# Performance work log

Hardware: AMD Instinct MI355X
Metric: run time of the kernel (lower is better)

## Reference

```python
import jax, jax.numpy as jnp
import numpy as np

HOP = 512
FAC = 4
FRAME_LEN = FAC * HOP  # 2048
ALPHA = 0.65
BETA = 0.06


def _inverse_stft_window():
    # torch.hann_window (periodic): w[n] = 0.5*(1 - cos(2*pi*n/N))
    n = np.arange(FRAME_LEN)
    w = 0.5 * (1.0 - np.cos(2.0 * np.pi * n / FRAME_LEN))
    denom = w ** 2
    # overlaps = ceil(frame_length / hop) == FAC (frame_length = FAC*HOP exactly)
    denom = denom.reshape(FAC, HOP).sum(axis=0)          # [HOP]
    denom = np.tile(denom, FAC)                          # [FRAME_LEN]
    return (w / denom).astype(np.float32)


def setup_inputs() -> dict:
    key = jax.random.key(0)
    B, F, T = 8, 1024, 2048
    stft_frames = jax.random.normal(key, (B, 2, F, T), dtype=jnp.float32)
    inv_window = jnp.asarray(_inverse_stft_window())
    return {"stft_frames": stft_frames, "inv_window": inv_window}


def reference(stft_frames, inv_window):
    # stft_frames: [B, 2, F, T] (real/imag stacked on dim 1)
    x = jnp.pad(stft_frames, ((0, 0), (0, 0), (0, 1), (0, 0)))  # F -> F+1 (Nyquist bin)
    real = x[:, 0] / BETA   # [B, F+1, T]
    imag = x[:, 1] / BETA
    # denormalize_complex: |x|^(1/alpha) * exp(i * atan2(im, re))
    mag = (real * real + imag * imag) ** (0.5 / ALPHA)
    theta = jnp.arctan2(imag, real)
    spec = jax.lax.complex(mag * jnp.cos(theta), mag * jnp.sin(theta))  # [B, F+1, T]
    frames = jnp.fft.irfft(spec, axis=-2)                 # [B, 2F, T], 2F == FRAME_LEN
    frames = jnp.transpose(frames, (0, 2, 1))             # [B, T, L]
    frames = frames * inv_window[None, None, :]
    B, T, L = frames.shape
    total = (T - 1) * HOP + L
    # vectorized overlap-add (scatter-add replacing the per-frame python loop)
    idx = (jnp.arange(T)[:, None] * HOP + jnp.arange(L)[None, :]).reshape(-1)  # [T*L]
    full = jnp.zeros((B, total), frames.dtype).at[:, idx].add(frames.reshape(B, -1))
    # output_buffer is empty on the first call; chunk = first hop*T samples
    return full[:, : HOP * T]
```

## Files before the change

kernel.cpp:

```cpp
#include <hip/hip_runtime.h>
#include <cstddef>


#define TDIM 2048
#define FDIM 1024
#define TT 8
#define NTOT (512 * 2048)
#define SPLANE 4224

static constexpr int kBREV[32] = {0,16,8,24,4,20,12,28,2,18,10,26,6,22,14,30,
                                  1,17,9,25,5,21,13,29,3,19,11,27,7,23,15,31};
static constexpr float kTR[16] = {
  1.0f, 0.98078528040323044f, 0.92387953251128674f, 0.83146961230254524f,
  0.70710678118654757f, 0.55557023301960218f, 0.38268343236508978f, 0.19509032201612825f,
  0.0f, -0.19509032201612825f, -0.38268343236508978f, -0.55557023301960218f,
  -0.70710678118654757f, -0.83146961230254524f, -0.92387953251128674f, -0.98078528040323044f};
static constexpr float kTI[16] = {
  0.0f, 0.19509032201612825f, 0.38268343236508978f, 0.55557023301960218f,
  0.70710678118654757f, 0.83146961230254524f, 0.92387953251128674f, 0.98078528040323044f,
  1.0f, 0.98078528040323044f, 0.92387953251128674f, 0.83146961230254524f,
  0.70710678118654757f, 0.55557023301960218f, 0.38268343236508978f, 0.19509032201612825f};
static constexpr float kCC[32] = {
  1.0f, 0.99518472667219693f, 0.98078528040323044f, 0.95694033573220882f,
  0.92387953251128674f, 0.88192126434835505f, 0.83146961230254524f, 0.77301045336273699f,
  0.70710678118654757f, 0.63439328416364549f, 0.55557023301960218f, 0.47139673682599764f,
  0.38268343236508978f, 0.29028467725446233f, 0.19509032201612825f, 0.098017140329560604f,
  0.0f, -0.098017140329560604f, -0.19509032201612825f, -0.29028467725446233f,
  -0.38268343236508978f, -0.47139673682599764f, -0.55557023301960218f, -0.63439328416364549f,
  -0.70710678118654757f, -0.77301045336273699f, -0.83146961230254524f, -0.88192126434835505f,
  -0.92387953251128674f, -0.95694033573220882f, -0.98078528040323044f, -0.99518472667219693f};
static constexpr float kSS[32] = {
  0.0f, 0.098017140329560604f, 0.19509032201612825f, 0.29028467725446233f,
  0.38268343236508978f, 0.47139673682599764f, 0.55557023301960218f, 0.63439328416364549f,
  0.70710678118654757f, 0.77301045336273699f, 0.83146961230254524f, 0.88192126434835505f,
  0.92387953251128674f, 0.95694033573220882f, 0.98078528040323044f, 0.99518472667219693f,
  1.0f, 0.99518472667219693f, 0.98078528040323044f, 0.95694033573220882f,
  0.92387953251128674f, 0.88192126434835505f, 0.83146961230254524f, 0.77301045336273699f,
  0.70710678118654757f, 0.63439328416364549f, 0.55557023301960218f, 0.47139673682599764f,
  0.38268343236508978f, 0.29028467725446233f, 0.19509032201612825f, 0.098017140329560604f};

template <int H>
__device__ __forceinline__ void fft32_stage(float ar[32], float ai[32]) {
  constexpr int TSTEP = 16 / H;
  #pragma unroll
  for (int g = 0; g < 32; g += 2 * H) {
    #pragma unroll
    for (int j = 0; j < H; ++j) {
      const float twr = kTR[j * TSTEP];
      const float twi = kTI[j * TSTEP];
      const int i0 = g + j, i1 = i0 + H;
      const float tr = twr * ar[i1] - twi * ai[i1];
      const float ti = twr * ai[i1] + twi * ar[i1];
      ar[i1] = ar[i0] - tr; ai[i1] = ai[i0] - ti;
      ar[i0] += tr;         ai[i0] += ti;
    }
  }
}

__device__ __forceinline__ void ifft32_core(float ar[32], float ai[32]) {
  fft32_stage<1>(ar, ai);
  fft32_stage<2>(ar, ai);
  fft32_stage<4>(ar, ai);
  fft32_stage<8>(ar, ai);
  fft32_stage<16>(ar, ai);
}

__device__ __forceinline__ float pow_gain(float v, float PE, float KS) {
  return KS * __builtin_amdgcn_exp2f(PE * __builtin_amdgcn_logf(v));
}

__device__ __forceinline__ void denorm4(float4& r, float4& i, float PE, float KS) {
  float g;
  g = pow_gain(r.x * r.x + i.x * i.x, PE, KS); r.x *= g; i.x *= g;
  g = pow_gain(r.y * r.y + i.y * i.y, PE, KS); r.y *= g; i.y *= g;
  g = pow_gain(r.z * r.z + i.z * i.z, PE, KS); r.z *= g; i.z *= g;
  g = pow_gain(r.w * r.w + i.w * i.w, PE, KS); r.w *= g; i.w *= g;
}

template <int SC>
__device__ __forceinline__ int slot_row(int s) {
  return (SC == 0) ? (s < 256 ? s : s + 512) : (s + 256);
}

template <int SC>
__device__ __forceinline__ void stage1_compute(const float* __restrict__ Sre,
                                               const float* __restrict__ Sim,
                                               int q, int tl, float wc, float ws,
                                               float ar[32], float ai[32]) {
  #pragma unroll
  for (int u = 0; u < 16; ++u) {
    const int k2 = (SC == 0) ? (u < 8 ? u : u + 16) : (u + 8);
    const int slot = q + 32 * u;
    int slotm_zero = 32 * (16 - u);
    if (SC == 0 && u == 0) slotm_zero = 0;
    if (SC == 0 && u == 8) slotm_zero = 512;
    const int slotm_pos = (32 - q) + 32 * (15 - u);
    const int slotm = (q == 0) ? slotm_zero : slotm_pos;

    const float s1r = Sre[slot * 8 + tl],  s1i = Sim[slot * 8 + tl];
    const float s2r = Sre[slotm * 8 + tl], s2i = Sim[slotm * 8 + tl];
    const float cs = wc * kCC[k2] - ws * kSS[k2];
    const float sn = ws * kCC[k2] + wc * kSS[k2];
    const float Pre = s1r + s2r, Pim = s1i - s2i;
    const float Qre = s1r - s2r, Qim = s1i + s2i;
    const float uu = cs * Qim + sn * Qre;
    const float vv = cs * Qre - sn * Qim;
    float wr = Pre - uu, wi = Pim + vv;
    if (q == 0 && k2 == 0) { wr = s1r; wi = s1r; }
    ar[kBREV[k2]] = wr; ai[kBREV[k2]] = wi;
  }
}

#define XH(t, k1, rh) ((k1) * 132 + (rh) * 8 + (t))
#define FSTR 2053

__global__ __launch_bounds__(256) void istft_fused(const float* __restrict__ in,
                                                   const float* __restrict__ invw,
                                                   float* __restrict__ out) {
  __shared__ float buf[8448];
  float* Sre = buf;
  float* Sim = buf + SPLANE;
  float* Xhr = buf;
  float* Xhi = buf + 4224;
  float* Fh  = buf;

  const int tid = threadIdx.x;
  const int tl  = tid & 7;
  const int q   = tid >> 3;

  const int id   = blockIdx.x;
  const int xcd  = id & 7;
  const int slot = id >> 3;
  const int b    = slot >> 5;
  const int tile = xcd * 32 + (slot & 31);
  const int t0   = tile * TT;

  const float* re_p = in + ((size_t)b * 2 + 0) * ((size_t)FDIM * TDIM);
  const float* im_p = in + ((size_t)b * 2 + 1) * ((size_t)FDIM * TDIM);

  const float KS = (float)(exp((-1.0 / 0.65) * log(0.06)) / 2048.0);
  const float PE = 7.0f / 26.0f;

  const float aq = 3.0679615757712824e-3f * (float)q;
  const float wc = __cosf(aq), ws = __sinf(aq);

  float ar[32], ai[32];

  float4 reA[4], imA[4];
  #pragma unroll
  for (int j = 0; j < 4; ++j) {
    const int f = tid + 256 * j;
    const int s = f >> 1, cg = f & 1;
    const int row = slot_row<0>(s);
    reA[j] = *(const float4*)(re_p + (size_t)row * TDIM + t0 + 4 * cg);
    imA[j] = *(const float4*)(im_p + (size_t)row * TDIM + t0 + 4 * cg);
  }
  float4 exRe, exIm;
  if (tid < 2) {
    exRe = *(const float4*)(re_p + (size_t)256 * TDIM + t0 + 4 * tid);
    exIm = *(const float4*)(im_p + (size_t)256 * TDIM + t0 + 4 * tid);
  }
  #pragma unroll
  for (int j = 0; j < 4; ++j) {
    const int f = tid + 256 * j;
    const int s = f >> 1, cg = f & 1;
    denorm4(reA[j], imA[j], PE, KS);
    *(float4*)(Sre + s * 8 + 4 * cg) = reA[j];
    *(float4*)(Sim + s * 8 + 4 * cg) = imA[j];
  }
  if (tid < 2) {
    denorm4(exRe, exIm, PE, KS);
    *(float4*)(Sre + 512 * 8 + 4 * tid) = exRe;
    *(float4*)(Sim + 512 * 8 + 4 * tid) = exIm;
  }

  float4 reB[4], imB[4];
  #pragma unroll
  for (int j = 0; j < 4; ++j) {
    const int f = tid + 256 * j;
    const int s = f >> 1, cg = f & 1;
    const int row = slot_row<1>(s);
    reB[j] = *(const float4*)(re_p + (size_t)row * TDIM + t0 + 4 * cg);
    imB[j] = *(const float4*)(im_p + (size_t)row * TDIM + t0 + 4 * cg);
  }
  float4 exReB, exImB;
  if (tid < 2) {
    exReB = *(const float4*)(re_p + (size_t)768 * TDIM + t0 + 4 * tid);
    exImB = *(const float4*)(im_p + (size_t)768 * TDIM + t0 + 4 * tid);
  }
  __syncthreads();

  stage1_compute<0>(Sre, Sim, q, tl, wc, ws, ar, ai);
  __syncthreads();

  #pragma unroll
  for (int j = 0; j < 4; ++j) {
    const int f = tid + 256 * j;
    const int s = f >> 1, cg = f & 1;
    denorm4(reB[j], imB[j], PE, KS);
    *(float4*)(Sre + s * 8 + 4 * cg) = reB[j];
    *(float4*)(Sim + s * 8 + 4 * cg) = imB[j];
  }
  if (tid < 2) {
    denorm4(exReB, exImB, PE, KS);
    *(float4*)(Sre + 512 * 8 + 4 * tid) = exReB;
    *(float4*)(Sim + 512 * 8 + 4 * tid) = exImB;
  }
  __syncthreads();
  stage1_compute<1>(Sre, Sim, q, tl, wc, ws, ar, ai);
  __syncthreads();

  ifft32_core(ar, ai);

  float zr[32], zi[32];
  #pragma unroll
  for (int r = 0; r < 16; ++r) {
    const float ang = 6.1359231515425649e-3f * (float)(q * r);
    const float sn = __sinf(ang), cs = __cosf(ang);
    Xhr[XH(tl, q, r)] = cs * ar[r] - sn * ai[r];
    Xhi[XH(tl, q, r)] = cs * ai[r] + sn * ar[r];
  }
  __syncthreads();
  if (q < 16) {
    #pragma unroll
    for (int i = 0; i < 32; ++i) {
      zr[i] = Xhr[XH(tl, kBREV[i], q)];
      zi[i] = Xhi[XH(tl, kBREV[i], q)];
    }
  }
  __syncthreads();
  #pragma unroll
  for (int r = 16; r < 32; ++r) {
    const float ang = 6.1359231515425649e-3f * (float)(q * r);
    const float sn = __sinf(ang), cs = __cosf(ang);
    Xhr[XH(tl, q, r - 16)] = cs * ar[r] - sn * ai[r];
    Xhi[XH(tl, q, r - 16)] = cs * ai[r] + sn * ar[r];
  }
  __syncthreads();
  if (q >= 16) {
    #pragma unroll
    for (int i = 0; i < 32; ++i) {
      zr[i] = Xhr[XH(tl, kBREV[i], q - 16)];
      zi[i] = Xhi[XH(tl, kBREV[i], q - 16)];
    }
  }
  __syncthreads();

  ifft32_core(zr, zi);

  float* ob = out + (size_t)b * NTOT;
  float acc[3][2];

  if (tl < 4) {
    #pragma unroll
    for (int s = 0; s < 32; ++s) {
      const int l0 = 2 * q + 64 * s;
      Fh[tl * FSTR + l0]     = zr[s] * invw[l0];
      Fh[tl * FSTR + l0 + 1] = zi[s] * invw[l0 + 1];
    }
  }
  __syncthreads();
  #pragma unroll
  for (int rel = 0; rel < 7; ++rel) {
    #pragma unroll
    for (int half = 0; half < 2; ++half) {
      const int j = tid + 256 * half;
      float v = 0.0f;
      #pragma unroll
      for (int c = 0; c < 4; ++c) {
        const int tt = rel - c;
        if (tt >= 0 && tt < 4) v += Fh[tt * FSTR + j + 512 * c];
      }
      if (rel < 3)       atomicAdd(&ob[(t0 + rel) * 512 + j], v);
      else if (rel == 3) ob[(t0 + rel) * 512 + j] = v;
      else               acc[rel - 4][half] = v;
    }
  }
  __syncthreads();
  if (tl >= 4) {
    #pragma unroll
    for (int s = 0; s < 32; ++s) {
      const int l0 = 2 * q + 64 * s;
      Fh[(tl - 4) * FSTR + l0]     = zr[s] * invw[l0];
      Fh[(tl - 4) * FSTR + l0 + 1] = zi[s] * invw[l0 + 1];
    }
  }
  __syncthreads();
  #pragma unroll
  for (int rel = 4; rel < 11; ++rel) {
    const int tp = t0 + rel;
    if (tp > 2047) continue;
    #pragma unroll
    for (int half = 0; half < 2; ++half) {
      const int j = tid + 256 * half;
      float v = (rel < 7) ? acc[rel - 4][half] : 0.0f;
      #pragma unroll
      for (int c = 0; c < 4; ++c) {
        const int tt = rel - c;
        if (tt >= 4 && tt < 8) v += Fh[(tt - 4) * FSTR + j + 512 * c];
      }
      const int n = tp * 512 + j;
      if (rel <= 7) ob[n] = v;
      else atomicAdd(&ob[n], v);
    }
  }
}

extern "C" void kernel_launch(void* const* d_in, const int* in_sizes, int n_in,
                              void* d_out, int out_size, void* d_ws, size_t ws_size,
                              hipStream_t stream) {
  (void)in_sizes; (void)n_in; (void)d_ws; (void)ws_size;
  const float* in   = (const float*)d_in[0];
  const float* invw = (const float*)d_in[1];
  float* out = (float*)d_out;
  hipMemsetAsync(out, 0, (size_t)out_size * sizeof(float), stream);
  istft_fused<<<dim3(TDIM / TT * 8), 256, 0, stream>>>(in, invw, out);
}
```

Baseline: 227.8 us.

## Double shared buffer to do transpose and overlap-add in single passes

Doubles the shared-memory buffer so the mid-FFT transpose and the windowed overlap-add staging each happen in one pass instead of two halves. This removes several barriers and the split register accumulators. The per-element twiddle sin/cos calls are replaced by an incremental rotation recurrence, and window loads and shared stores are vectorised as float2. The larger LDS footprint (about 66 KB per block) may reduce blocks per CU. The recurrence also adds small accumulated rounding error.

```diff
diff --git a/kernel.cpp b/kernel.cpp
--- a/kernel.cpp
+++ b/kernel.cpp
@@ -111,17 +111,17 @@
   }
 }
 
-#define XH(t, k1, rh) ((k1) * 132 + (rh) * 8 + (t))
-#define FSTR 2053
+#define XIDX(t, k1, r) ((k1) * 264 + (r) * 8 + (t))
+#define FSTR 2054
 
 __global__ __launch_bounds__(256) void istft_fused(const float* __restrict__ in,
                                                    const float* __restrict__ invw,
                                                    float* __restrict__ out) {
-  __shared__ float buf[8448];
+  __shared__ float buf[16896];
   float* Sre = buf;
   float* Sim = buf + SPLANE;
-  float* Xhr = buf;
-  float* Xhi = buf + 4224;
+  float* Xr  = buf;
+  float* Xi  = buf + 8448;
   float* Fh  = buf;
 
   const int tid = threadIdx.x;
@@ -146,122 +146,111 @@
 
   float ar[32], ai[32];
 
-  float4 reA[4], imA[4];
-  #pragma unroll
-  for (int j = 0; j < 4; ++j) {
-    const int f = tid + 256 * j;
-    const int s = f >> 1, cg = f & 1;
-    const int row = slot_row<0>(s);
-    reA[j] = *(const float4*)(re_p + (size_t)row * TDIM + t0 + 4 * cg);
-    imA[j] = *(const float4*)(im_p + (size_t)row * TDIM + t0 + 4 * cg);
-  }
-  float4 exRe, exIm;
-  if (tid < 2) {
-    exRe = *(const float4*)(re_p + (size_t)256 * TDIM + t0 + 4 * tid);
-    exIm = *(const float4*)(im_p + (size_t)256 * TDIM + t0 + 4 * tid);
-  }
-  #pragma unroll
-  for (int j = 0; j < 4; ++j) {
-    const int f = tid + 256 * j;
-    const int s = f >> 1, cg = f & 1;
-    denorm4(reA[j], imA[j], PE, KS);
-    *(float4*)(Sre + s * 8 + 4 * cg) = reA[j];
-    *(float4*)(Sim + s * 8 + 4 * cg) = imA[j];
-  }
-  if (tid < 2) {
-    denorm4(exRe, exIm, PE, KS);
-    *(float4*)(Sre + 512 * 8 + 4 * tid) = exRe;
-    *(float4*)(Sim + 512 * 8 + 4 * tid) = exIm;
-  }
-
-  float4 reB[4], imB[4];
-  #pragma unroll
-  for (int j = 0; j < 4; ++j) {
-    const int f = tid + 256 * j;
-    const int s = f >> 1, cg = f & 1;
-    const int row = slot_row<1>(s);
-    reB[j] = *(const float4*)(re_p + (size_t)row * TDIM + t0 + 4 * cg);
-    imB[j] = *(const float4*)(im_p + (size_t)row * TDIM + t0 + 4 * cg);
-  }
-  float4 exReB, exImB;
-  if (tid < 2) {
-    exReB = *(const float4*)(re_p + (size_t)768 * TDIM + t0 + 4 * tid);
-    exImB = *(const float4*)(im_p + (size_t)768 * TDIM + t0 + 4 * tid);
+  {
+    float4 reA[4], imA[4];
+    #pragma unroll
+    for (int j = 0; j < 4; ++j) {
+      const int f = tid + 256 * j;
+      const int s = f >> 1, cg = f & 1;
+      const int row = slot_row<0>(s);
+      reA[j] = *(const float4*)(re_p + (size_t)row * TDIM + t0 + 4 * cg);
+      imA[j] = *(const float4*)(im_p + (size_t)row * TDIM + t0 + 4 * cg);
+    }
+    float4 exRe, exIm;
+    if (tid < 2) {
+      exRe = *(const float4*)(re_p + (size_t)256 * TDIM + t0 + 4 * tid);
+      exIm = *(const float4*)(im_p + (size_t)256 * TDIM + t0 + 4 * tid);
+    }
+    #pragma unroll
+    for (int j = 0; j < 4; ++j) {
+      const int f = tid + 256 * j;
+      const int s = f >> 1, cg = f & 1;
+      denorm4(reA[j], imA[j], PE, KS);
+      *(float4*)(Sre + s * 8 + 4 * cg) = reA[j];
+      *(float4*)(Sim + s * 8 + 4 * cg) = imA[j];
+    }
+    if (tid < 2) {
+      denorm4(exRe, exIm, PE, KS);
+      *(float4*)(Sre + 512 * 8 + 4 * tid) = exRe;
+      *(float4*)(Sim + 512 * 8 + 4 * tid) = exIm;
+    }
+
+    float4 reB[4], imB[4];
+    #pragma unroll
+    for (int j = 0; j < 4; ++j) {
+      const int f = tid + 256 * j;
+      const int s = f >> 1, cg = f & 1;
+      const int row = slot_row<1>(s);
+      reB[j] = *(const float4*)(re_p + (size_t)row * TDIM + t0 + 4 * cg);
+      imB[j] = *(const float4*)(im_p + (size_t)row * TDIM + t0 + 4 * cg);
+    }
+    float4 exReB, exImB;
+    if (tid < 2) {
+      exReB = *(const float4*)(re_p + (size_t)768 * TDIM + t0 + 4 * tid);
+      exImB = *(const float4*)(im_p + (size_t)768 * TDIM + t0 + 4 * tid);
+    }
+    __syncthreads();
+
+    stage1_compute<0>(Sre, Sim, q, tl, wc, ws, ar, ai);
+    __syncthreads();
+
+    #pragma unroll
+    for (int j = 0; j < 4; ++j) {
+      const int f = tid + 256 * j;
+      const int s = f >> 1, cg = f & 1;
+      denorm4(reB[j], imB[j], PE, KS);
+      *(float4*)(Sre + s * 8 + 4 * cg) = reB[j];
+      *(float4*)(Sim + s * 8 + 4 * cg) = imB[j];
+    }
+    if (tid < 2) {
+      denorm4(exReB, exImB, PE, KS);
+      *(float4*)(Sre + 512 * 8 + 4 * tid) = exReB;
+      *(float4*)(Sim + 512 * 8 + 4 * tid) = exImB;
+    }
+    __syncthreads();
+    stage1_compute<1>(Sre, Sim, q, tl, wc, ws, ar, ai);
+    __syncthreads();
+  }
+
+  ifft32_core(ar, ai);
+
+  {
+    const float aq2 = 6.1359231515425649e-3f * (float)q;
+    const float dc = __cosf(aq2), dsn = __sinf(aq2);
+    float cs = 1.0f, sn = 0.0f;
+    #pragma unroll
+    for (int r = 0; r < 32; ++r) {
+      Xr[XIDX(tl, q, r)] = cs * ar[r] - sn * ai[r];
+      Xi[XIDX(tl, q, r)] = cs * ai[r] + sn * ar[r];
+      const float ncs = cs * dc - sn * dsn;
+      sn = cs * dsn + sn * dc;
+      cs = ncs;
+    }
   }
   __syncthreads();
-
-  stage1_compute<0>(Sre, Sim, q, tl, wc, ws, ar, ai);
+  float zr[32], zi[32];
+  #pragma unroll
+  for (int i = 0; i < 32; ++i) {
+    zr[i] = Xr[XIDX(tl, kBREV[i], q)];
+    zi[i] = Xi[XIDX(tl, kBREV[i], q)];
+  }
   __syncthreads();
 
-  #pragma unroll
-  for (int j = 0; j < 4; ++j) {
-    const int f = tid + 256 * j;
-    const int s = f >> 1, cg = f & 1;
-    denorm4(reB[j], imB[j], PE, KS);
-    *(float4*)(Sre + s * 8 + 4 * cg) = reB[j];
-    *(float4*)(Sim + s * 8 + 4 * cg) = imB[j];
-  }
-  if (tid < 2) {
-    denorm4(exReB, exImB, PE, KS);
-    *(float4*)(Sre + 512 * 8 + 4 * tid) = exReB;
-    *(float4*)(Sim + 512 * 8 + 4 * tid) = exImB;
+  ifft32_core(zr, zi);
+
+  #pragma unroll
+  for (int s = 0; s < 32; ++s) {
+    const int l0 = 2 * q + 64 * s;
+    const float2 w2 = *(const float2*)(invw + l0);
+    float2 fv; fv.x = zr[s] * w2.x; fv.y = zi[s] * w2.y;
+    *(float2*)(Fh + tl * FSTR + l0) = fv;
   }
   __syncthreads();
-  stage1_compute<1>(Sre, Sim, q, tl, wc, ws, ar, ai);
-  __syncthreads();
-
-  ifft32_core(ar, ai);
-
-  float zr[32], zi[32];
-  #pragma unroll
-  for (int r = 0; r < 16; ++r) {
-    const float ang = 6.1359231515425649e-3f * (float)(q * r);
-    const float sn = __sinf(ang), cs = __cosf(ang);
-    Xhr[XH(tl, q, r)] = cs * ar[r] - sn * ai[r];
-    Xhi[XH(tl, q, r)] = cs * ai[r] + sn * ar[r];
-  }
-  __syncthreads();
-  if (q < 16) {
-    #pragma unroll
-    for (int i = 0; i < 32; ++i) {
-      zr[i] = Xhr[XH(tl, kBREV[i], q)];
-      zi[i] = Xhi[XH(tl, kBREV[i], q)];
-    }
-  }
-  __syncthreads();
-  #pragma unroll
-  for (int r = 16; r < 32; ++r) {
-    const float ang = 6.1359231515425649e-3f * (float)(q * r);
-    const float sn = __sinf(ang), cs = __cosf(ang);
-    Xhr[XH(tl, q, r - 16)] = cs * ar[r] - sn * ai[r];
-    Xhi[XH(tl, q, r - 16)] = cs * ai[r] + sn * ar[r];
-  }
-  __syncthreads();
-  if (q >= 16) {
-    #pragma unroll
-    for (int i = 0; i < 32; ++i) {
-      zr[i] = Xhr[XH(tl, kBREV[i], q - 16)];
-      zi[i] = Xhi[XH(tl, kBREV[i], q - 16)];
-    }
-  }
-  __syncthreads();
-
-  ifft32_core(zr, zi);
 
   float* ob = out + (size_t)b * NTOT;
-  float acc[3][2];
-
-  if (tl < 4) {
-    #pragma unroll
-    for (int s = 0; s < 32; ++s) {
-      const int l0 = 2 * q + 64 * s;
-      Fh[tl * FSTR + l0]     = zr[s] * invw[l0];
-      Fh[tl * FSTR + l0 + 1] = zi[s] * invw[l0 + 1];
-    }
-  }
-  __syncthreads();
-  #pragma unroll
-  for (int rel = 0; rel < 7; ++rel) {
+  for (int rel = 0; rel < 11; ++rel) {
+    const int tp = t0 + rel;
+    if (tp > 2047) break;
     #pragma unroll
     for (int half = 0; half < 2; ++half) {
       const int j = tid + 256 * half;
@@ -269,38 +258,10 @@
       #pragma unroll
       for (int c = 0; c < 4; ++c) {
         const int tt = rel - c;
-        if (tt >= 0 && tt < 4) v += Fh[tt * FSTR + j + 512 * c];
-      }
-      if (rel < 3)       atomicAdd(&ob[(t0 + rel) * 512 + j], v);
-      else if (rel == 3) ob[(t0 + rel) * 512 + j] = v;
-      else               acc[rel - 4][half] = v;
-    }
-  }
-  __syncthreads();
-  if (tl >= 4) {
-    #pragma unroll
-    for (int s = 0; s < 32; ++s) {
-      const int l0 = 2 * q + 64 * s;
-      Fh[(tl - 4) * FSTR + l0]     = zr[s] * invw[l0];
-      Fh[(tl - 4) * FSTR + l0 + 1] = zi[s] * invw[l0 + 1];
-    }
-  }
-  __syncthreads();
-  #pragma unroll
-  for (int rel = 4; rel < 11; ++rel) {
-    const int tp = t0 + rel;
-    if (tp > 2047) continue;
-    #pragma unroll
-    for (int half = 0; half < 2; ++half) {
-      const int j = tid + 256 * half;
-      float v = (rel < 7) ? acc[rel - 4][half] : 0.0f;
-      #pragma unroll
-      for (int c = 0; c < 4; ++c) {
-        const int tt = rel - c;
-        if (tt >= 4 && tt < 8) v += Fh[(tt - 4) * FSTR + j + 512 * c];
+        if (tt >= 0 && tt < TT) v += Fh[tt * FSTR + j + 512 * c];
       }
       const int n = tp * 512 + j;
-      if (rel <= 7) ob[n] = v;
+      if (rel >= 3 && rel <= 7) ob[n] = v;
       else atomicAdd(&ob[n], v);
     }
   }
```

Result: no change. 229.6 us (+0.8%).
